# Kernel tuning notes

Measured on AMD Instinct MI355X. Metric: run time of the kernel, lower is better.

Reference implementation:

```python
import jax, jax.numpy as jnp
import numpy as np

T, B, S = 128, 128, 128
H, E, V, L = 1024, 512, 32000, 2


def setup_inputs() -> dict:
    key = jax.random.key(0)
    ks = jax.random.split(key, 16)
    s = 0.02
    inp = {
        "inputs": jax.random.randint(ks[0], (T, B), 0, V),
        "h0": jax.random.normal(ks[1], (L, B, H), jnp.float32) * 0.1,
        "c0": jax.random.normal(ks[2], (L, B, H), jnp.float32) * 0.1,
        "contexts": jax.random.normal(ks[3], (B, S, H), jnp.float32),
        "emb": jax.random.normal(ks[4], (V, E), jnp.float32) * s,
        "W_ih0": jax.random.normal(ks[5], (4 * H, E), jnp.float32) * s,
        "W_hh0": jax.random.normal(ks[6], (4 * H, H), jnp.float32) * s,
        "b_ih0": jnp.zeros((4 * H,), jnp.float32),
        "b_hh0": jnp.zeros((4 * H,), jnp.float32),
        "W_ih1": jax.random.normal(ks[7], (4 * H, H), jnp.float32) * s,
        "W_hh1": jax.random.normal(ks[8], (4 * H, H), jnp.float32) * s,
        "b_ih1": jnp.zeros((4 * H,), jnp.float32),
        "b_hh1": jnp.zeros((4 * H,), jnp.float32),
        "att_in_W": jax.random.normal(ks[9], (H, H), jnp.float32) * s,
        "att_in_b": jnp.zeros((H,), jnp.float32),
        "att_out_W": jax.random.normal(ks[10], (H, 2 * H), jnp.float32) * s,
        "att_out_b": jnp.zeros((H,), jnp.float32),
    }
    return inp


def _lstm_cell(x, h, c, Wih, Whh, bih, bhh):
    # torch.nn.LSTMCell: gates in (i, f, g, o) order
    gates = x @ Wih.T + bih + h @ Whh.T + bhh  # [B, 4H]
    i, f, g, o = jnp.split(gates, 4, axis=-1)
    c2 = jax.nn.sigmoid(f) * c + jax.nn.sigmoid(i) * jnp.tanh(g)
    h2 = jax.nn.sigmoid(o) * jnp.tanh(c2)
    return h2, c2


def reference(inputs, h0, c0, contexts, emb,
              W_ih0, W_hh0, b_ih0, b_hh0,
              W_ih1, W_hh1, b_ih1, b_hh1,
              att_in_W, att_in_b, att_out_W, att_out_b):
    layer_params = [(W_ih0, W_hh0, b_ih0, b_hh0), (W_ih1, W_hh1, b_ih1, b_hh1)]
    embs = emb[inputs]  # [T, B, E]

    def step(carry, x_t):
        h, c = carry  # each [L, B, H]
        x = x_t
        hs, cs = [], []
        for l, (Wih, Whh, bih, bhh) in enumerate(layer_params):
            h_l, c_l = _lstm_cell(x, h[l], c[l], Wih, Whh, bih, bhh)
            x = h_l  # dropout=0.0 / eval mode -> identity
            hs.append(h_l)
            cs.append(c_l)
        # global (Luong general) attention
        gamma = x @ att_in_W.T + att_in_b                     # [B, H]
        scores = jnp.einsum('bsh,bh->bs', contexts, gamma)    # [B, S]
        w = jax.nn.softmax(scores, axis=-1)
        c_t = jnp.einsum('bs,bsh->bh', w, contexts)           # [B, H]
        out = jnp.tanh(jnp.concatenate([c_t, x], axis=-1) @ att_out_W.T + att_out_b)
        return (jnp.stack(hs), jnp.stack(cs)), (out, w)

    (hT, cT), (outputs, attns) = jax.lax.scan(step, (h0, c0), embs)
    return outputs, hT, cT
```

## Files before the change

kernel.cpp:

```cpp
#include <hip/hip_runtime.h>

#define TT 128
#define BB 128
#define SS 128
#define HH 1024
#define EE 512
#define BH (BB*HH)

typedef unsigned short u16;
typedef __attribute__((ext_vector_type(8))) short s8v;
typedef __attribute__((ext_vector_type(4))) float f32x4;

__device__ __forceinline__ float b2f(u16 u) {
    union { unsigned int i; float f; } v; v.i = ((unsigned int)u) << 16; return v.f;
}
__device__ __forceinline__ u16 f2b(float f) {
    union { float f; unsigned int i; } v; v.f = f;
    unsigned int x = v.i;
    x = x + 0x7fffu + ((x >> 16) & 1u);
    return (u16)(x >> 16);
}
__device__ __forceinline__ float sigm(float x) {
    float t = __expf(-fabsf(x));
    float p = 1.0f / (1.0f + t);
    return x >= 0.0f ? p : 1.0f - p;
}
__device__ __forceinline__ float tanh_(float x) {
    float t = __expf(-2.0f * fabsf(x));
    float r = (1.0f - t) / (1.0f + t);
    return x >= 0.0f ? r : -r;
}

#define MFMA(a, b, c) __builtin_amdgcn_mfma_f32_16x16x32_bf16((a), (b), (c), 0, 0, 0)

__global__ __launch_bounds__(256)
void cvt_k(const float* __restrict__ s, u16* __restrict__ d, int n)
{
    const int i = (blockIdx.x * 256 + threadIdx.x) * 4;
    if (i < n) {
        const float4 v = *(const float4*)(s + i);
        ushort4 o;
        o.x = f2b(v.x); o.y = f2b(v.y); o.z = f2b(v.z); o.w = f2b(v.w);
        *(ushort4*)(d + i) = o;
    }
}

__global__ __launch_bounds__(128)
void gather_k(const int* __restrict__ toks, const float* __restrict__ emb,
              u16* __restrict__ X)
{
    const int row = blockIdx.x;
    const int tok = toks[row];
    const int c = threadIdx.x * 4;
    const float4 v = *(const float4*)(emb + (size_t)tok * EE + c);
    ushort4 o;
    o.x = f2b(v.x); o.y = f2b(v.y); o.z = f2b(v.z); o.w = f2b(v.w);
    *(ushort4*)(X + (size_t)row * EE + c) = o;
}

__global__ __launch_bounds__(256)
void init_k(const float* __restrict__ h0in,
            u16* __restrict__ h0ring, u16* __restrict__ h1init,
            int* __restrict__ barcnt)
{
    const int i = blockIdx.x * 256 + threadIdx.x;
    const u16 hb = f2b(h0in[i]);
    if (i < BH) h0ring[i] = hb;
    else        h1init[i - BH] = hb;
    if (i == 0) *barcnt = 0;
}

__global__ __launch_bounds__(512, 1)
void scan_k(const float* __restrict__ Wih0, const float* __restrict__ Whh0,
            const float* __restrict__ Wih1, const float* __restrict__ Whh1,
            const float* __restrict__ bih0, const float* __restrict__ bhh0,
            const float* __restrict__ bih1, const float* __restrict__ bhh1,
            const float* __restrict__ c0in,
            const u16* __restrict__ Xb,
            u16* __restrict__ h0ring,
            const u16* __restrict__ h1init,
            u16* __restrict__ H1all,
            float* __restrict__ outT,
            int* __restrict__ barcnt)
{
    extern __shared__ u16 lds[];
    u16* W0x = lds;
    u16* W0h = W0x + 16*4*16*8;
    u16* W1x = W0h + 32*4*16*8;
    u16* W1h = W1x + 32*4*16*8;
    float* gst0 = (float*)(W1h + 32*4*16*8);
    float* gst1 = gst0 + 8*16*20;

    const int tid  = threadIdx.x;
    const int bk   = blockIdx.x;
    const int j0   = (((bk & 7) << 5) | (bk >> 3)) * 4;
    const int lane = tid & 63;
    const int w    = tid >> 6;
    const int l15  = lane & 15, quad = lane >> 4;

    auto loadW = [&](const float* src, int K, u16* dst) {
        const int ntup = (K / 32) * 4 * 16;
        for (int idx = tid; idx < ntup; idx += 512) {
            const int n = idx & 15, q = (idx >> 4) & 3, kc = idx >> 6;
            const int col = ((n >> 2) * HH) + j0 + (n & 3);
            const float* sp = src + (size_t)col * K + kc * 32 + q * 8;
            const float4 v0 = *(const float4*)(sp);
            const float4 v1 = *(const float4*)(sp + 4);
            u16* dp = dst + (size_t)idx * 8;
            dp[0] = f2b(v0.x); dp[1] = f2b(v0.y); dp[2] = f2b(v0.z); dp[3] = f2b(v0.w);
            dp[4] = f2b(v1.x); dp[5] = f2b(v1.y); dp[6] = f2b(v1.z); dp[7] = f2b(v1.w);
        }
    };
    loadW(Wih0, EE, W0x);
    loadW(Whh0, HH, W0h);
    loadW(Wih1, HH, W1x);
    loadW(Whh1, HH, W1h);

    const int prow = tid >> 2;
    const int pjj  = tid & 3;
    const int pj   = j0 + pjj;
    const int pw   = prow >> 4, pr16 = prow & 15;

    float c0 = c0in[(size_t)0 * BH + (size_t)prow * HH + pj];
    float c1 = c0in[(size_t)1 * BH + (size_t)prow * HH + pj];
    float b0[4], b1[4];
    #pragma unroll
    for (int g = 0; g < 4; ++g) {
        b0[g] = bih0[g * HH + pj] + bhh0[g * HH + pj];
        b1[g] = bih1[g * HH + pj] + bhh1[g * HH + pj];
    }

    __syncthreads();

    const int arow = w * 16 + l15;

    #define BIDX(kc) (((size_t)((kc) * 4 + quad) * 16 + l15) * 8)

    for (int p = 0; p <= TT; ++p) {
        f32x4 acc0 = (f32x4)0.0f, acc1 = (f32x4)0.0f;

        if (p < TT) {
            const u16* ap = Xb + ((size_t)p * BB + arow) * EE + quad * 8;
            #pragma unroll 8
            for (int kc = 0; kc < 16; ++kc) {
                s8v a = *(const s8v*)(ap + kc * 32);
                s8v b = *(const s8v*)(W0x + BIDX(kc));
                acc0 = MFMA(a, b, acc0);
            }
        }

        if (p > 0) {
            if (tid == 0) {
                const int target = 256 * p;
                while (__hip_atomic_load(barcnt, __ATOMIC_RELAXED,
                                         __HIP_MEMORY_SCOPE_AGENT) < target) {
                    __builtin_amdgcn_s_sleep(2);
                }
            }
            __syncthreads();
            asm volatile("" ::: "memory");
        }

        const u16* h0p = h0ring + (size_t)p * BH;
        const u16* a0p = h0p + (size_t)arow * HH + quad * 8;
        if (p == 0) {
            #pragma unroll 8
            for (int kc = 0; kc < 32; ++kc) {
                s8v a = *(const s8v*)(a0p + kc * 32);
                acc0 = MFMA(a, *(const s8v*)(W0h + BIDX(kc)), acc0);
            }
        } else {
            const u16* h1p = (p == 1) ? h1init : (H1all + (size_t)(p - 2) * BH);
            const u16* a1p = h1p + (size_t)arow * HH + quad * 8;
            if (p < TT) {
                #pragma unroll 8
                for (int kc = 0; kc < 32; ++kc) {
                    s8v a0 = *(const s8v*)(a0p + kc * 32);
                    s8v a1 = *(const s8v*)(a1p + kc * 32);
                    acc0 = MFMA(a0, *(const s8v*)(W0h + BIDX(kc)), acc0);
                    acc1 = MFMA(a0, *(const s8v*)(W1x + BIDX(kc)), acc1);
                    acc1 = MFMA(a1, *(const s8v*)(W1h + BIDX(kc)), acc1);
                }
            } else {
                #pragma unroll 8
                for (int kc = 0; kc < 32; ++kc) {
                    s8v a0 = *(const s8v*)(a0p + kc * 32);
                    s8v a1 = *(const s8v*)(a1p + kc * 32);
                    acc1 = MFMA(a0, *(const s8v*)(W1x + BIDX(kc)), acc1);
                    acc1 = MFMA(a1, *(const s8v*)(W1h + BIDX(kc)), acc1);
                }
            }
        }

        if (p < TT) {
            #pragma unroll
            for (int r = 0; r < 4; ++r)
                gst0[w * 320 + (quad * 4 + r) * 20 + l15] = acc0[r];
        }
        if (p > 0) {
            #pragma unroll
            for (int r = 0; r < 4; ++r)
                gst1[w * 320 + (quad * 4 + r) * 20 + l15] = acc1[r];
        }
        __syncthreads();
        if (p < TT) {
            const float* gr = gst0 + pw * 320 + pr16 * 20;
            const float gi = gr[0 + pjj]  + b0[0];
            const float gf = gr[4 + pjj]  + b0[1];
            const float gg = gr[8 + pjj]  + b0[2];
            const float go = gr[12 + pjj] + b0[3];
            c0 = sigm(gf) * c0 + sigm(gi) * tanh_(gg);
            const float h = sigm(go) * tanh_(c0);
            h0ring[(size_t)(p + 1) * BH + (size_t)prow * HH + pj] = f2b(h);
            if (p == TT - 1) {
                outT[(size_t)0 * BH + (size_t)prow * HH + pj] = h;
                outT[(size_t)2 * BH + (size_t)prow * HH + pj] = c0;
            }
        }
        if (p > 0) {
            const float* gr = gst1 + pw * 320 + pr16 * 20;
            const float gi = gr[0 + pjj]  + b1[0];
            const float gf = gr[4 + pjj]  + b1[1];
            const float gg = gr[8 + pjj]  + b1[2];
            const float go = gr[12 + pjj] + b1[3];
            c1 = sigm(gf) * c1 + sigm(gi) * tanh_(gg);
            const float h = sigm(go) * tanh_(c1);
            H1all[(size_t)(p - 1) * BH + (size_t)prow * HH + pj] = f2b(h);
            if (p == TT) {
                outT[(size_t)1 * BH + (size_t)prow * HH + pj] = h;
                outT[(size_t)3 * BH + (size_t)prow * HH + pj] = c1;
            }
        }
        __syncthreads();

        if (p < TT && tid == 0) {
            __hip_atomic_fetch_add(barcnt, 1, __ATOMIC_RELEASE,
                                   __HIP_MEMORY_SCOPE_AGENT);
        }
    }
    #undef BIDX
}

__global__ __launch_bounds__(256)
void gemm_bt_k(const u16* __restrict__ A1, int K1,
               const u16* __restrict__ A2, int K2,
               const u16* __restrict__ W, int ldw,
               const float* __restrict__ bias,
               u16* __restrict__ Cb, float* __restrict__ Cf,
               int N, int act)
{
    const int lane = threadIdx.x & 63;
    const int wave = threadIdx.x >> 6;
    const int l15 = lane & 15, quad = lane >> 4;
    const int n0 = blockIdx.x * 64;
    const int mrow = blockIdx.y * 64 + wave * 16;
    const int arow = mrow + l15;

    f32x4 acc[4];
    #pragma unroll
    for (int nt = 0; nt < 4; ++nt) acc[nt] = (f32x4)0.0f;

    const u16* wr0 = W + (size_t)(n0 + 0 * 16 + l15) * ldw + quad * 8;
    const u16* wr1 = W + (size_t)(n0 + 1 * 16 + l15) * ldw + quad * 8;
    const u16* wr2 = W + (size_t)(n0 + 2 * 16 + l15) * ldw + quad * 8;
    const u16* wr3 = W + (size_t)(n0 + 3 * 16 + l15) * ldw + quad * 8;

    {
        const u16* ap = A1 + (size_t)arow * K1 + quad * 8;
        #pragma unroll 4
        for (int kk = 0; kk < K1; kk += 32) {
            s8v a = *(const s8v*)(ap + kk);
            acc[0] = MFMA(a, *(const s8v*)(wr0 + kk), acc[0]);
            acc[1] = MFMA(a, *(const s8v*)(wr1 + kk), acc[1]);
            acc[2] = MFMA(a, *(const s8v*)(wr2 + kk), acc[2]);
            acc[3] = MFMA(a, *(const s8v*)(wr3 + kk), acc[3]);
        }
    }
    if (A2 != nullptr) {
        const u16* ap = A2 + (size_t)arow * K2 + quad * 8;
        #pragma unroll 4
        for (int kk = 0; kk < K2; kk += 32) {
            s8v a = *(const s8v*)(ap + kk);
            acc[0] = MFMA(a, *(const s8v*)(wr0 + K1 + kk), acc[0]);
            acc[1] = MFMA(a, *(const s8v*)(wr1 + K1 + kk), acc[1]);
            acc[2] = MFMA(a, *(const s8v*)(wr2 + K1 + kk), acc[2]);
            acc[3] = MFMA(a, *(const s8v*)(wr3 + K1 + kk), acc[3]);
        }
    }
    #pragma unroll
    for (int nt = 0; nt < 4; ++nt) {
        const int col = n0 + nt * 16 + l15;
        const float bv = bias[col];
        #pragma unroll
        for (int r = 0; r < 4; ++r) {
            const int row = mrow + quad * 4 + r;
            float v = acc[nt][r] + bv;
            if (act) v = tanh_(v);
            if (Cf) Cf[(size_t)row * N + col] = v;
            else    Cb[(size_t)row * N + col] = f2b(v);
        }
    }
}

__global__ __launch_bounds__(256)
void attn_k(const u16* __restrict__ gamma, const float* __restrict__ ctx,
            u16* __restrict__ ctall)
{
    const int b = blockIdx.x;
    const int t0 = blockIdx.y * 16;
    const int tid = threadIdx.x;
    const int lane = tid & 63, wave = tid >> 6;
    const int l15 = lane & 15, quad = lane >> 4;

    __shared__ float sw[16 * SS];

    {
        f32x4 acc0 = (f32x4)0.0f, acc1 = (f32x4)0.0f;
        const u16*   ap  = gamma + ((size_t)(t0 + l15) * BB + b) * HH + quad * 8;
        const float* bp0 = ctx + ((size_t)b * SS + (wave * 32 + l15)) * HH + quad * 8;
        const float* bp1 = ctx + ((size_t)b * SS + (wave * 32 + 16 + l15)) * HH + quad * 8;
        for (int kk = 0; kk < HH; kk += 32) {
            s8v a = *(const s8v*)(ap + kk);
            float4 u0 = *(const float4*)(bp0 + kk);
            float4 u1 = *(const float4*)(bp0 + kk + 4);
            s8v bv;
            bv[0] = (short)f2b(u0.x); bv[1] = (short)f2b(u0.y);
            bv[2] = (short)f2b(u0.z); bv[3] = (short)f2b(u0.w);
            bv[4] = (short)f2b(u1.x); bv[5] = (short)f2b(u1.y);
            bv[6] = (short)f2b(u1.z); bv[7] = (short)f2b(u1.w);
            acc0 = MFMA(a, bv, acc0);
            float4 w0 = *(const float4*)(bp1 + kk);
            float4 w1 = *(const float4*)(bp1 + kk + 4);
            s8v cv;
            cv[0] = (short)f2b(w0.x); cv[1] = (short)f2b(w0.y);
            cv[2] = (short)f2b(w0.z); cv[3] = (short)f2b(w0.w);
            cv[4] = (short)f2b(w1.x); cv[5] = (short)f2b(w1.y);
            cv[6] = (short)f2b(w1.z); cv[7] = (short)f2b(w1.w);
            acc1 = MFMA(a, cv, acc1);
        }
        #pragma unroll
        for (int r = 0; r < 4; ++r) {
            const int trow = quad * 4 + r;
            sw[trow * SS + wave * 32 + l15] = acc0[r];
            sw[trow * SS + wave * 32 + 16 + l15] = acc1[r];
        }
    }
    __syncthreads();

    {
        const int row = tid >> 4, c0 = tid & 15;
        float e[8];
        float m = -1e30f;
        #pragma unroll
        for (int k = 0; k < 8; ++k) { e[k] = sw[row * SS + c0 + k * 16]; m = fmaxf(m, e[k]); }
        #pragma unroll
        for (int off = 8; off >= 1; off >>= 1) m = fmaxf(m, __shfl_xor(m, off));
        float s = 0.0f;
        #pragma unroll
        for (int k = 0; k < 8; ++k) { e[k] = __expf(e[k] - m); s += e[k]; }
        #pragma unroll
        for (int off = 8; off >= 1; off >>= 1) s += __shfl_xor(s, off);
        const float inv = 1.0f / s;
        #pragma unroll
        for (int k = 0; k < 8; ++k) sw[row * SS + c0 + k * 16] = e[k] * inv;
    }
    __syncthreads();

    {
        const int h0 = tid * 4;
        float a[16][4];
        #pragma unroll
        for (int t = 0; t < 16; ++t)
            #pragma unroll
            for (int q = 0; q < 4; ++q) a[t][q] = 0.0f;

        const float* cp = ctx + (size_t)b * SS * HH + h0;
        for (int s = 0; s < SS; ++s) {
            const float4 cv = *(const float4*)(cp + (size_t)s * HH);
            #pragma unroll
            for (int t = 0; t < 16; ++t) {
                const float wgt = sw[t * SS + s];
                a[t][0] += wgt * cv.x;
                a[t][1] += wgt * cv.y;
                a[t][2] += wgt * cv.z;
                a[t][3] += wgt * cv.w;
            }
        }
        #pragma unroll
        for (int t = 0; t < 16; ++t) {
            u16* op = ctall + ((size_t)(t0 + t) * BB + b) * HH + h0;
            #pragma unroll
            for (int q = 0; q < 4; ++q) op[q] = f2b(a[t][q]);
        }
    }
}

extern "C" void kernel_launch(void* const* d_in, const int* in_sizes, int n_in,
                              void* d_out, int out_size, void* d_ws, size_t ws_size,
                              hipStream_t stream)
{
    const int*   toks = (const int*)d_in[0];
    const float* h0in = (const float*)d_in[1];
    const float* c0in = (const float*)d_in[2];
    const float* ctx  = (const float*)d_in[3];
    const float* emb  = (const float*)d_in[4];
    const float* Wih0 = (const float*)d_in[5];
    const float* Whh0 = (const float*)d_in[6];
    const float* bih0 = (const float*)d_in[7];
    const float* bhh0 = (const float*)d_in[8];
    const float* Wih1 = (const float*)d_in[9];
    const float* Whh1 = (const float*)d_in[10];
    const float* bih1 = (const float*)d_in[11];
    const float* bhh1 = (const float*)d_in[12];
    const float* attW = (const float*)d_in[13];
    const float* attb = (const float*)d_in[14];
    const float* outW = (const float*)d_in[15];
    const float* outb = (const float*)d_in[16];

    u16*   h0ring = (u16*)d_ws;
    u16*   h1init = h0ring + (size_t)(TT + 1) * BH;
    int*   barcnt = (int*)(h1init + BH);
    u16*   Xb     = (u16*)(barcnt + 64);
    u16*   H1all  = Xb + (size_t)TT * BB * EE;
    u16*   gammaA = H1all + (size_t)TT * BH;
    u16*   attWb  = gammaA + (size_t)TT * BH;
    u16*   outWb  = attWb + (size_t)HH * HH;
    u16*   ctall  = h0ring;

    cvt_k<<<dim3((HH * HH / 4 + 255) / 256), 256, 0, stream>>>(attW, attWb, HH * HH);
    cvt_k<<<dim3((2 * HH * HH / 4 + 255) / 256), 256, 0, stream>>>(outW, outWb, 2 * HH * HH);

    gather_k<<<dim3(TT * BB), 128, 0, stream>>>(toks, emb, Xb);
    init_k<<<dim3(2 * BH / 256), 256, 0, stream>>>(h0in, h0ring, h1init, barcnt);

    float* outp = (float*)d_out;
    const int ldsBytes = (16*4*16*8 + 3 * 32*4*16*8) * 2 + 2 * 8*16*20 * 4;
    hipFuncSetAttribute((const void*)scan_k,
                        hipFuncAttributeMaxDynamicSharedMemorySize, ldsBytes);
    scan_k<<<dim3(256), 512, ldsBytes, stream>>>(
        Wih0, Whh0, Wih1, Whh1, bih0, bhh0, bih1, bhh1, c0in,
        Xb, h0ring, h1init, H1all, outp + (size_t)TT * BH, barcnt);

    gemm_bt_k<<<dim3(HH / 64, (TT * BB) / 64), 256, 0, stream>>>(
        H1all, HH, nullptr, 0, attWb, HH, attb, gammaA, nullptr, HH, 0);

    attn_k<<<dim3(BB, TT / 16), 256, 0, stream>>>(gammaA, ctx, ctall);

    gemm_bt_k<<<dim3(HH / 64, (TT * BB) / 64), 256, 0, stream>>>(
        ctall, HH, H1all, HH, outWb, 2 * HH, outb, nullptr, outp, HH, 1);
}
```

Measured before the change: 4.264 ms.

## Shard grid barrier counter and vectorize LSTM pointwise with packed atomic stores

Splits the single global barrier counter into 8 padded counters, so arrivals contend less and 8 threads poll in parallel with a shorter sleep. The release fetch-add becomes relaxed and the h stores become relaxed agent-scope 64-bit atomic stores. The LSTM pointwise step now has 128 threads per layer each handle 4 columns with vector LDS loads, instead of 512 threads each doing one column. Relaxing the release ordering risks memory-visibility bugs across blocks, and concentrating the pointwise work on fewer threads lengthens that phase per thread.

```diff
diff --git a/kernel.cpp b/kernel.cpp
--- a/kernel.cpp
+++ b/kernel.cpp
@@ -8,6 +8,7 @@
 #define BH (BB*HH)
 
 typedef unsigned short u16;
+typedef unsigned long long u64;
 typedef __attribute__((ext_vector_type(8))) short s8v;
 typedef __attribute__((ext_vector_type(4))) float f32x4;
 
@@ -67,7 +68,7 @@
     const u16 hb = f2b(h0in[i]);
     if (i < BH) h0ring[i] = hb;
     else        h1init[i - BH] = hb;
-    if (i == 0) *barcnt = 0;
+    if (i < 256) barcnt[i] = 0;
 }
 
 __global__ __launch_bounds__(512, 1)
@@ -116,18 +117,18 @@
     loadW(Wih1, HH, W1x);
     loadW(Whh1, HH, W1h);
 
-    const int prow = tid >> 2;
-    const int pjj  = tid & 3;
-    const int pj   = j0 + pjj;
-    const int pw   = prow >> 4, pr16 = prow & 15;
-
-    float c0 = c0in[(size_t)0 * BH + (size_t)prow * HH + pj];
-    float c1 = c0in[(size_t)1 * BH + (size_t)prow * HH + pj];
-    float b0[4], b1[4];
-    #pragma unroll
-    for (int g = 0; g < 4; ++g) {
-        b0[g] = bih0[g * HH + pj] + bhh0[g * HH + pj];
-        b1[g] = bih1[g * HH + pj] + bhh1[g * HH + pj];
+    const int pr = tid & 127;
+    f32x4 cst = (f32x4)0.0f;
+    f32x4 bs0 = (f32x4)0.0f, bs1 = (f32x4)0.0f, bs2 = (f32x4)0.0f, bs3 = (f32x4)0.0f;
+    if (tid < 256) {
+        const int layer = tid >> 7;
+        const float* bi = layer ? bih1 : bih0;
+        const float* bh = layer ? bhh1 : bhh0;
+        cst = *(const f32x4*)(c0in + (size_t)layer * BH + (size_t)pr * HH + j0);
+        bs0 = *(const f32x4*)(bi + 0 * HH + j0) + *(const f32x4*)(bh + 0 * HH + j0);
+        bs1 = *(const f32x4*)(bi + 1 * HH + j0) + *(const f32x4*)(bh + 1 * HH + j0);
+        bs2 = *(const f32x4*)(bi + 2 * HH + j0) + *(const f32x4*)(bh + 2 * HH + j0);
+        bs3 = *(const f32x4*)(bi + 3 * HH + j0) + *(const f32x4*)(bh + 3 * HH + j0);
     }
 
     __syncthreads();
@@ -135,6 +136,34 @@
     const int arow = w * 16 + l15;
 
     #define BIDX(kc) (((size_t)((kc) * 4 + quad) * 16 + l15) * 8)
+
+    auto pointwise = [&](const float* gbase, u16* dst, float* oH, float* oC,
+                         bool doOut) {
+        const float* gr = gbase + (pr >> 4) * 320 + (pr & 15) * 20;
+        const f32x4 vi = *(const f32x4*)(gr + 0);
+        const f32x4 vf = *(const f32x4*)(gr + 4);
+        const f32x4 vg = *(const f32x4*)(gr + 8);
+        const f32x4 vo = *(const f32x4*)(gr + 12);
+        f32x4 hv;
+        #pragma unroll
+        for (int jj = 0; jj < 4; ++jj) {
+            const float gi = vi[jj] + bs0[jj];
+            const float gf = vf[jj] + bs1[jj];
+            const float gg = vg[jj] + bs2[jj];
+            const float go = vo[jj] + bs3[jj];
+            const float c = sigm(gf) * cst[jj] + sigm(gi) * tanh_(gg);
+            cst[jj] = c;
+            hv[jj] = sigm(go) * tanh_(c);
+        }
+        const u64 pk = (u64)f2b(hv[0]) | ((u64)f2b(hv[1]) << 16)
+                     | ((u64)f2b(hv[2]) << 32) | ((u64)f2b(hv[3]) << 48);
+        __hip_atomic_store((u64*)(dst + (size_t)pr * HH + j0), pk,
+                           __ATOMIC_RELAXED, __HIP_MEMORY_SCOPE_AGENT);
+        if (doOut) {
+            *(f32x4*)(oH + (size_t)pr * HH + j0) = hv;
+            *(f32x4*)(oC + (size_t)pr * HH + j0) = cst;
+        }
+    };
 
     for (int p = 0; p <= TT; ++p) {
         f32x4 acc0 = (f32x4)0.0f, acc1 = (f32x4)0.0f;
@@ -150,11 +179,11 @@
         }
 
         if (p > 0) {
-            if (tid == 0) {
-                const int target = 256 * p;
-                while (__hip_atomic_load(barcnt, __ATOMIC_RELAXED,
+            if (tid < 8) {
+                const int target = 32 * p;
+                while (__hip_atomic_load(barcnt + tid * 32, __ATOMIC_RELAXED,
                                          __HIP_MEMORY_SCOPE_AGENT) < target) {
-                    __builtin_amdgcn_s_sleep(2);
+                    __builtin_amdgcn_s_sleep(1);
                 }
             }
             __syncthreads();
@@ -203,38 +232,16 @@
                 gst1[w * 320 + (quad * 4 + r) * 20 + l15] = acc1[r];
         }
         __syncthreads();
-        if (p < TT) {
-            const float* gr = gst0 + pw * 320 + pr16 * 20;
-            const float gi = gr[0 + pjj]  + b0[0];
-            const float gf = gr[4 + pjj]  + b0[1];
-            const float gg = gr[8 + pjj]  + b0[2];
-            const float go = gr[12 + pjj] + b0[3];
-            c0 = sigm(gf) * c0 + sigm(gi) * tanh_(gg);
-            const float h = sigm(go) * tanh_(c0);
-            h0ring[(size_t)(p + 1) * BH + (size_t)prow * HH + pj] = f2b(h);
-            if (p == TT - 1) {
-                outT[(size_t)0 * BH + (size_t)prow * HH + pj] = h;
-                outT[(size_t)2 * BH + (size_t)prow * HH + pj] = c0;
-            }
-        }
-        if (p > 0) {
-            const float* gr = gst1 + pw * 320 + pr16 * 20;
-            const float gi = gr[0 + pjj]  + b1[0];
-            const float gf = gr[4 + pjj]  + b1[1];
-            const float gg = gr[8 + pjj]  + b1[2];
-            const float go = gr[12 + pjj] + b1[3];
-            c1 = sigm(gf) * c1 + sigm(gi) * tanh_(gg);
-            const float h = sigm(go) * tanh_(c1);
-            H1all[(size_t)(p - 1) * BH + (size_t)prow * HH + pj] = f2b(h);
-            if (p == TT) {
-                outT[(size_t)1 * BH + (size_t)prow * HH + pj] = h;
-                outT[(size_t)3 * BH + (size_t)prow * HH + pj] = c1;
-            }
-        }
+        if (p < TT && tid < 128)
+            pointwise(gst0, h0ring + (size_t)(p + 1) * BH,
+                      outT + (size_t)0 * BH, outT + (size_t)2 * BH, p == TT - 1);
+        if (p > 0 && tid >= 128 && tid < 256)
+            pointwise(gst1, H1all + (size_t)(p - 1) * BH,
+                      outT + (size_t)1 * BH, outT + (size_t)3 * BH, p == TT);
         __syncthreads();
 
         if (p < TT && tid == 0) {
-            __hip_atomic_fetch_add(barcnt, 1, __ATOMIC_RELEASE,
+            __hip_atomic_fetch_add(barcnt + (bk & 7) * 32, 1, __ATOMIC_RELAXED,
                                    __HIP_MEMORY_SCOPE_AGENT);
         }
     }
@@ -420,7 +427,7 @@
     u16*   h0ring = (u16*)d_ws;
     u16*   h1init = h0ring + (size_t)(TT + 1) * BH;
     int*   barcnt = (int*)(h1init + BH);
-    u16*   Xb     = (u16*)(barcnt + 64);
+    u16*   Xb     = (u16*)(barcnt + 256);
     u16*   H1all  = Xb + (size_t)TT * BB * EE;
     u16*   gammaA = H1all + (size_t)TT * BH;
     u16*   attWb  = gammaA + (size_t)TT * BH;
```

Result: faster. 3.706 ms (-13.1%).
